# Kernel optimization log

Hardware: AMD Instinct MI355X
Metric: run time of the kernel (lower is better)

## Reference

```python
import jax, jax.numpy as jnp
import numpy as np

N, NFEAT, NHID, NCLASS, NHEADS, E = 4096, 512, 64, 40, 4, 131072
ALPHA = 0.2
NEG = -9e15


def _gat_head(W, b, a, ab, h, adj):
    # Faithful to attention(cat[Wh_i, Wh_j]) but computed without the N*N*2F
    # concat: a . [Wh_i, Wh_j] + ab = (Wh_i . a_src) + (Wh_j . a_dst) + ab
    Wh = h @ W + b                          # [N, F]
    F2 = Wh.shape[1]
    src = Wh @ a[:F2]                       # [N]
    dst = Wh @ a[F2:]                       # [N]
    e = jax.nn.leaky_relu(src[:, None] + dst[None, :] + ab, negative_slope=ALPHA)
    e = jnp.where(adj, e, NEG)              # masked scores [N, N]
    att = jax.nn.softmax(e, axis=1)
    return att @ Wh                         # [N, F]


def setup_inputs() -> dict:
    key = jax.random.key(0)
    ks = jax.random.split(key, 10)
    x = jax.random.normal(ks[0], (N, NFEAT), dtype=jnp.float32)
    edge_index = jax.random.randint(ks[1], (2, E), 0, N, dtype=jnp.int64)
    s = 0.05
    W1 = jax.random.normal(ks[2], (NHEADS, NFEAT, NHID), dtype=jnp.float32) * s
    b1 = jax.random.normal(ks[3], (NHEADS, NHID), dtype=jnp.float32) * s
    a1 = jax.random.normal(ks[4], (NHEADS, 2 * NHID), dtype=jnp.float32) * s
    ab1 = jax.random.normal(ks[5], (NHEADS,), dtype=jnp.float32) * s
    Wo = jax.random.normal(ks[6], (NHEADS * NHID, NCLASS), dtype=jnp.float32) * s
    bo = jax.random.normal(ks[7], (NCLASS,), dtype=jnp.float32) * s
    ao = jax.random.normal(ks[8], (2 * NCLASS,), dtype=jnp.float32) * s
    abo = jax.random.normal(ks[9], (), dtype=jnp.float32) * s
    return {"x": x, "edge_index": edge_index, "W1": W1, "b1": b1, "a1": a1,
            "ab1": ab1, "Wo": Wo, "bo": bo, "ao": ao, "abo": abo}


def reference(x, edge_index, W1, b1, a1, ab1, Wo, bo, ao, abo):
    # dense adjacency from edge list (to_dense_adj equivalent)
    adj = jnp.zeros((N, N), dtype=bool).at[edge_index[0], edge_index[1]].set(True)
    # first multi-head layer (concat=True -> elu per head, then concat)
    hs = jax.vmap(_gat_head, in_axes=(0, 0, 0, 0, None, None))(
        W1, b1, a1, ab1, x, adj)            # [H, N, NHID]
    h = jax.nn.elu(hs)
    h = jnp.transpose(h, (1, 0, 2)).reshape(N, NHEADS * NHID)
    # output head (concat=False), then outer elu + log_softmax
    out = _gat_head(Wo, bo, ao, abo, h, adj)  # [N, NCLASS]
    out = jax.nn.elu(out)
    return jax.nn.log_softmax(out, axis=1)
```

## Files before the change

kernel.cpp:

```cpp
#include <hip/hip_runtime.h>
#include <cstdint>
#include <cstddef>

#define N_NODES 4096
#define NFEAT   512
#define NHID    64
#define NCLASS  40
#define NHEADS  4
#define ALPHA_S 0.2f
#define MAXD    96

typedef __bf16 bf16x8 __attribute__((ext_vector_type(8)));
typedef float  f32x4  __attribute__((ext_vector_type(4)));

__device__ __forceinline__ float lrelu(float x) { return x > 0.f ? x : ALPHA_S * x; }

__device__ __forceinline__ unsigned short f2bf(float f) {
    unsigned u = __float_as_uint(f);
    u += 0x7fffu + ((u >> 16) & 1u);
    return (unsigned short)(u >> 16);
}

__device__ __forceinline__ float wredmax(float m) {
    #pragma unroll
    for (int o = 32; o; o >>= 1) m = fmaxf(m, __shfl_xor(m, o));
    return m;
}
__device__ __forceinline__ float wredsum(float s) {
    #pragma unroll
    for (int o = 32; o; o >>= 1) s += __shfl_xor(s, o);
    return s;
}

__global__ __launch_bounds__(256) void prep(const float* __restrict__ x,
                                            const int* __restrict__ ei, int E,
                                            const float* __restrict__ W1,
                                            const float* __restrict__ Wo,
                                            unsigned short* __restrict__ xb,
                                            unsigned short* __restrict__ Bt,
                                            unsigned short* __restrict__ Wot,
                                            int* __restrict__ cnt,
                                            unsigned short* __restrict__ nbr_raw) {
    const int u = blockIdx.x, tid = threadIdx.x;
    if (u < 1024) {
        size_t idx = (size_t)u * 2048 + tid * 8;
        float4 v0 = *reinterpret_cast<const float4*>(x + idx);
        float4 v1 = *reinterpret_cast<const float4*>(x + idx + 4);
        uint4 o;
        o.x = (unsigned)f2bf(v0.x) | ((unsigned)f2bf(v0.y) << 16);
        o.y = (unsigned)f2bf(v0.z) | ((unsigned)f2bf(v0.w) << 16);
        o.z = (unsigned)f2bf(v1.x) | ((unsigned)f2bf(v1.y) << 16);
        o.w = (unsigned)f2bf(v1.z) | ((unsigned)f2bf(v1.w) << 16);
        *reinterpret_cast<uint4*>(xb + idx) = o;
    } else if (u < 1280) {
        int n = u - 1024;
        int h = n >> 6, c = n & 63;
        for (int k = tid; k < NFEAT; k += 256)
            Bt[(size_t)n * NFEAT + k] = f2bf(W1[(size_t)h * NFEAT * NHID + (size_t)k * NHID + c]);
    } else if (u < 1344) {
        int n = u - 1280;
        unsigned short v = 0;
        if (n < NCLASS) v = f2bf(Wo[(size_t)tid * NCLASS + n]);
        Wot[(size_t)n * 256 + tid] = v;
    } else {
        int t = (u - 1344) * 256 + tid;
        if (t < E) {
            int r = ei[t];
            int c = ei[E + t];
            int slot = atomicAdd(&cnt[r], 1);
            if (slot < MAXD) nbr_raw[(size_t)r * MAXD + slot] = (unsigned short)c;
        }
    }
}

__device__ __forceinline__ void gemm_tile(const unsigned short* __restrict__ Ab,
                                          const unsigned short* __restrict__ Bb,
                                          int K, unsigned short* As, unsigned short* Bs,
                                          f32x4 acc[2][2]) {
    const int tid = threadIdx.x;
    const int l = tid & 63;
    const int wid = tid >> 6;
    const int wr = wid >> 1, wc = wid & 1;
    int aoff[2][2], boff[2][2];
    #pragma unroll
    for (int f = 0; f < 2; ++f) {
        int r = wr * 32 + f * 16 + (l & 15);
        int c = wc * 32 + f * 16 + (l & 15);
        #pragma unroll
        for (int s = 0; s < 2; ++s) {
            int gk = (s << 2) + (l >> 4);
            aoff[f][s] = r * 64 + ((gk ^ (r & 7)) << 3);
            boff[f][s] = c * 64 + ((gk ^ (c & 7)) << 3);
        }
    }
    for (int k0 = 0; k0 < K; k0 += 64) {
        for (int g2 = tid; g2 < 512; g2 += 256) {
            int row = g2 >> 3, gc = g2 & 7;
            uint4 va = *reinterpret_cast<const uint4*>(Ab + (size_t)row * K + k0 + (gc << 3));
            *reinterpret_cast<uint4*>(As + row * 64 + ((gc ^ (row & 7)) << 3)) = va;
            uint4 vb = *reinterpret_cast<const uint4*>(Bb + (size_t)row * K + k0 + (gc << 3));
            *reinterpret_cast<uint4*>(Bs + row * 64 + ((gc ^ (row & 7)) << 3)) = vb;
        }
        __syncthreads();
        #pragma unroll
        for (int s = 0; s < 2; ++s) {
            bf16x8 av[2], bv[2];
            #pragma unroll
            for (int f = 0; f < 2; ++f) {
                av[f] = *reinterpret_cast<const bf16x8*>(As + aoff[f][s]);
                bv[f] = *reinterpret_cast<const bf16x8*>(Bs + boff[f][s]);
            }
            #pragma unroll
            for (int fa = 0; fa < 2; ++fa)
                #pragma unroll
                for (int fb = 0; fb < 2; ++fb)
                    acc[fa][fb] = __builtin_amdgcn_mfma_f32_16x16x32_bf16(
                        av[fa], bv[fb], acc[fa][fb], 0, 0, 0);
        }
        __syncthreads();
    }
}

union MidSMem {
    struct { unsigned short As[4096]; unsigned short Bs[4096]; } g;
    float stage[64][65];
    unsigned int bm[4][128];
};

__global__ __launch_bounds__(256) void mid(const unsigned short* __restrict__ xb,
                                           const unsigned short* __restrict__ Bt,
                                           const float* __restrict__ b1,
                                           const float* __restrict__ a1,
                                           const int* __restrict__ cnt,
                                           const unsigned short* __restrict__ nbr_raw,
                                           float* __restrict__ Wh1,
                                           float* __restrict__ src1,
                                           float* __restrict__ dst1,
                                           int* __restrict__ deg,
                                           unsigned short* __restrict__ nbr) {
    __shared__ MidSMem sm;
    const int tid = threadIdx.x;
    const int l = tid & 63;
    const int wid = tid >> 6;

    if (blockIdx.x < 256) {
        const int u = blockIdx.x;
        const int rt = u & 63, h = u >> 6;
        f32x4 acc[2][2] = {};
        gemm_tile(xb + (size_t)(rt * 64) * NFEAT, Bt + (size_t)(h * 64) * NFEAT,
                  NFEAT, sm.g.As, sm.g.Bs, acc);
        const int wr = wid >> 1, wc = wid & 1;
        #pragma unroll
        for (int fa = 0; fa < 2; ++fa)
            #pragma unroll
            for (int fb = 0; fb < 2; ++fb) {
                int col = wc * 32 + fb * 16 + (l & 15);
                float bias = b1[h * NHID + col];
                #pragma unroll
                for (int j = 0; j < 4; ++j) {
                    int row = wr * 32 + fa * 16 + ((l >> 4) << 2) + j;
                    float v = acc[fa][fb][j] + bias;
                    Wh1[((size_t)h * N_NODES + rt * 64 + row) * NHID + col] = v;
                    sm.stage[row][col] = v;
                }
            }
        __syncthreads();
        for (int rr = 0; rr < 16; ++rr) {
            int row = wid * 16 + rr;
            float v = sm.stage[row][l];
            float s = v * a1[h * 2 * NHID + l];
            float d2 = v * a1[h * 2 * NHID + NHID + l];
            s = wredsum(s); d2 = wredsum(d2);
            if (l == 0) {
                src1[h * N_NODES + rt * 64 + row] = s;
                dst1[h * N_NODES + rt * 64 + row] = d2;
            }
        }
    } else {
        int idx = blockIdx.x - 256;
        for (int u = idx; u < 1024; u += 768) {
            int i = u * 4 + wid;
            sm.bm[wid][2 * l] = 0;
            sm.bm[wid][2 * l + 1] = 0;
            __syncthreads();
            int dr = cnt[i]; if (dr > MAXD) dr = MAXD;
            for (int q = l; q < dr; q += 64) {
                int c = nbr_raw[(size_t)i * MAXD + q];
                atomicOr(&sm.bm[wid][c >> 5], 1u << (c & 31));
            }
            __syncthreads();
            unsigned long long wv = (unsigned long long)sm.bm[wid][2 * l]
                                  | ((unsigned long long)sm.bm[wid][2 * l + 1] << 32);
            int cpc = __popcll(wv);
            int pre = cpc;
            #pragma unroll
            for (int o = 1; o < 64; o <<= 1) {
                int v = __shfl_up(pre, o);
                if (l >= o) pre += v;
            }
            int total = __shfl(pre, 63);
            int basep = pre - cpc;
            if (l == 0) deg[i] = total;
            while (wv) {
                int b = __builtin_ctzll(wv); wv &= wv - 1;
                nbr[(size_t)i * MAXD + basep++] = (unsigned short)(l * 64 + b);
            }
            __syncthreads();
        }
    }
}

__global__ __launch_bounds__(256) void attn1(const float* __restrict__ Wh1,
                                             const float* __restrict__ src1,
                                             const float* __restrict__ dst1,
                                             const float* __restrict__ ab1,
                                             const int* __restrict__ deg,
                                             const unsigned short* __restrict__ nbr,
                                             unsigned short* __restrict__ hb) {
    __shared__ unsigned short nb[MAXD];
    __shared__ float ev[NHEADS][MAXD];
    const int i = blockIdx.x;
    const int tid = threadIdx.x;
    const int l = tid & 63;
    const int h = tid >> 6;
    const int d = deg[i];
    for (int q = tid; q < d; q += 256) nb[q] = nbr[(size_t)i * MAXD + q];
    __syncthreads();
    const float s_i = src1[h * N_NODES + i];
    const float ab = ab1[h];
    const float* __restrict__ dsth = dst1 + h * N_NODES;
    const float* __restrict__ Whh = Wh1 + (size_t)h * N_NODES * NHID;
    int j0 = (l < d) ? nb[l] : -1;
    int j1 = (l + 64 < d) ? nb[l + 64] : -1;
    float s0 = (j0 >= 0) ? lrelu(s_i + dsth[j0] + ab) : -1e30f;
    float s1 = (j1 >= 0) ? lrelu(s_i + dsth[j1] + ab) : -1e30f;
    float m = wredmax(fmaxf(s0, s1));
    float e0 = (j0 >= 0) ? __expf(s0 - m) : 0.f;
    float e1 = (j1 >= 0) ? __expf(s1 - m) : 0.f;
    if (j0 >= 0) ev[h][l] = e0;
    if (j1 >= 0) ev[h][l + 64] = e1;
    float lsum = wredsum(e0 + e1);
    float acc = 0.f;
    if (d == 0) {
        float s = 0.f;
        for (int j = 0; j < N_NODES; ++j) s += Whh[(size_t)j * NHID + l];
        acc = s * (1.f / N_NODES);
    } else {
        #pragma unroll 8
        for (int q = 0; q < d; ++q)
            acc += ev[h][q] * Whh[(size_t)nb[q] * NHID + l];
        acc *= (1.f / lsum);
    }
    float o = acc > 0.f ? acc : __expf(acc) - 1.f;
    hb[(size_t)i * (NHEADS * NHID) + h * NHID + l] = f2bf(o);
}

__global__ __launch_bounds__(256) void gemm2(const unsigned short* __restrict__ hb,
                                             const unsigned short* __restrict__ Wot,
                                             const float* __restrict__ bo,
                                             const float* __restrict__ ao,
                                             float* __restrict__ Who,
                                             float* __restrict__ srco,
                                             float* __restrict__ dsto) {
    __shared__ MidSMem sm;
    const int tid = threadIdx.x;
    const int l = tid & 63;
    const int wid = tid >> 6;
    const int rt = blockIdx.x;
    f32x4 acc[2][2] = {};
    gemm_tile(hb + (size_t)(rt * 64) * (NHEADS * NHID), Wot,
              NHEADS * NHID, sm.g.As, sm.g.Bs, acc);
    const int wr = wid >> 1, wc = wid & 1;
    #pragma unroll
    for (int fa = 0; fa < 2; ++fa)
        #pragma unroll
        for (int fb = 0; fb < 2; ++fb) {
            int col = wc * 32 + fb * 16 + (l & 15);
            if (col < NCLASS) {
                float bias = bo[col];
                #pragma unroll
                for (int j = 0; j < 4; ++j) {
                    int row = wr * 32 + fa * 16 + ((l >> 4) << 2) + j;
                    float v = acc[fa][fb][j] + bias;
                    Who[(size_t)(rt * 64 + row) * NCLASS + col] = v;
                    sm.stage[row][col] = v;
                }
            }
        }
    __syncthreads();
    for (int rr = 0; rr < 16; ++rr) {
        int row = wid * 16 + rr;
        float v = (l < NCLASS) ? sm.stage[row][l] : 0.f;
        float s = (l < NCLASS) ? v * ao[l] : 0.f;
        float d2 = (l < NCLASS) ? v * ao[NCLASS + l] : 0.f;
        s = wredsum(s); d2 = wredsum(d2);
        if (l == 0) {
            srco[rt * 64 + row] = s;
            dsto[rt * 64 + row] = d2;
        }
    }
}

__global__ __launch_bounds__(256) void attn2(const float* __restrict__ Who,
                                             const float* __restrict__ srco,
                                             const float* __restrict__ dsto,
                                             const float* __restrict__ abo_p,
                                             const int* __restrict__ deg,
                                             const unsigned short* __restrict__ nbr,
                                             float* __restrict__ out) {
    __shared__ unsigned short nb[4][MAXD];
    __shared__ float ev[4][MAXD];
    const int tid = threadIdx.x;
    const int wid = tid >> 6;
    const int l = tid & 63;
    const int i = blockIdx.x * 4 + wid;
    const int d = deg[i];
    unsigned short* nbw = nb[wid];
    for (int q = l; q < d; q += 64) nbw[q] = nbr[(size_t)i * MAXD + q];
    const float ab = abo_p[0];
    const float s_i = srco[i];
    int j0 = (l < d) ? nbw[l] : -1;
    int j1 = (l + 64 < d) ? nbw[l + 64] : -1;
    float s0 = (j0 >= 0) ? lrelu(s_i + dsto[j0] + ab) : -1e30f;
    float s1 = (j1 >= 0) ? lrelu(s_i + dsto[j1] + ab) : -1e30f;
    float m = wredmax(fmaxf(s0, s1));
    float e0 = (j0 >= 0) ? __expf(s0 - m) : 0.f;
    float e1 = (j1 >= 0) ? __expf(s1 - m) : 0.f;
    if (j0 >= 0) ev[wid][l] = e0;
    if (j1 >= 0) ev[wid][l + 64] = e1;
    float lsum = wredsum(e0 + e1);
    float acc = 0.f;
    if (d == 0) {
        if (l < NCLASS) {
            float s = 0.f;
            for (int j = 0; j < N_NODES; ++j) s += Who[(size_t)j * NCLASS + l];
            acc = s * (1.f / N_NODES);
        }
    } else if (l < NCLASS) {
        #pragma unroll 8
        for (int q = 0; q < d; ++q)
            acc += ev[wid][q] * Who[(size_t)nbw[q] * NCLASS + l];
        acc *= (1.f / lsum);
    }
    float v = acc > 0.f ? acc : __expf(acc) - 1.f;
    float xv = (l < NCLASS) ? v : -1e30f;
    float mx = wredmax(xv);
    float ex = (l < NCLASS) ? __expf(v - mx) : 0.f;
    ex = wredsum(ex);
    if (l < NCLASS) out[(size_t)i * NCLASS + l] = v - mx - logf(ex);
}

extern "C" void kernel_launch(void* const* d_in, const int* in_sizes, int n_in,
                              void* d_out, int out_size, void* d_ws, size_t ws_size,
                              hipStream_t stream) {
    const float* x   = (const float*)d_in[0];
    const int*   ei  = (const int*)d_in[1];
    const float* W1  = (const float*)d_in[2];
    const float* b1  = (const float*)d_in[3];
    const float* a1  = (const float*)d_in[4];
    const float* ab1 = (const float*)d_in[5];
    const float* Wo  = (const float*)d_in[6];
    const float* bo  = (const float*)d_in[7];
    const float* ao  = (const float*)d_in[8];
    const float* abo = (const float*)d_in[9];
    float* out = (float*)d_out;
    const int E = in_sizes[1] / 2;

    char* base = (char*)d_ws;
    const size_t MB = 1024 * 1024;
    int*            cnt     = (int*)(base);
    int*            deg     = (int*)(base + 16 * 1024);
    unsigned short* nbr_raw = (unsigned short*)(base + 32 * 1024);
    unsigned short* nbr     = (unsigned short*)(base + 32 * 1024 + 786432);
    unsigned short* xb      = (unsigned short*)(base + 2 * MB);
    unsigned short* Bt      = (unsigned short*)(base + 6 * MB);
    unsigned short* Wot     = (unsigned short*)(base + 6 * MB + 262144);
    float*          Wh1     = (float*)(base + 7 * MB);
    float*          src1    = (float*)(base + 11 * MB);
    float*          dst1    = (float*)(base + 11 * MB + 65536);
    unsigned short* hb      = (unsigned short*)(base + 12 * MB);
    float*          Who     = (float*)(base + 14 * MB);
    float*          srco    = (float*)(base + 15 * MB);
    float*          dsto    = (float*)(base + 15 * MB + 16384);

    hipMemsetAsync(cnt, 0, 16 * 1024, stream);
    prep<<<1856, 256, 0, stream>>>(x, ei, E, W1, Wo, xb, Bt, Wot, cnt, nbr_raw);
    mid<<<1024, 256, 0, stream>>>(xb, Bt, b1, a1, cnt, nbr_raw, Wh1, src1, dst1, deg, nbr);
    attn1<<<N_NODES, 256, 0, stream>>>(Wh1, src1, dst1, ab1, deg, nbr, hb);
    gemm2<<<64, 256, 0, stream>>>(hb, Wot, bo, ao, Who, srco, dsto);
    attn2<<<N_NODES / 4, 256, 0, stream>>>(Who, srco, dsto, abo, deg, nbr, out);
}
```

Before: 71.78 us.

## Replace neighbor-list staging with global adjacency bitmask built by atomicOr

Drops the per-row count/raw-neighbor arrays and the separate dedup/compaction pass. A 2 MB dense bitmask is zeroed in prep, and edges are scattered into it with 64-bit atomicOr inside mid, alongside the GEMM blocks. Both attention kernels then rebuild the sorted neighbor list from the bitmask with popcount prefix scans. attn1 also becomes a grid-stride loop over 1024 blocks, and prep handles 16 elements per thread. The cost is zeroing and reading a larger bitmask and repeating the compaction in both attention kernels. MAXD is raised to 128.

```diff
diff --git a/kernel.cpp b/kernel.cpp
--- a/kernel.cpp
+++ b/kernel.cpp
@@ -8,7 +8,7 @@
 #define NCLASS  40
 #define NHEADS  4
 #define ALPHA_S 0.2f
-#define MAXD    96
+#define MAXD    128
 
 typedef __bf16 bf16x8 __attribute__((ext_vector_type(8)));
 typedef float  f32x4  __attribute__((ext_vector_type(4)));
@@ -33,43 +33,40 @@
 }
 
 __global__ __launch_bounds__(256) void prep(const float* __restrict__ x,
-                                            const int* __restrict__ ei, int E,
                                             const float* __restrict__ W1,
                                             const float* __restrict__ Wo,
                                             unsigned short* __restrict__ xb,
                                             unsigned short* __restrict__ Bt,
                                             unsigned short* __restrict__ Wot,
-                                            int* __restrict__ cnt,
-                                            unsigned short* __restrict__ nbr_raw) {
+                                            uint4* __restrict__ adj4) {
     const int u = blockIdx.x, tid = threadIdx.x;
-    if (u < 1024) {
-        size_t idx = (size_t)u * 2048 + tid * 8;
-        float4 v0 = *reinterpret_cast<const float4*>(x + idx);
-        float4 v1 = *reinterpret_cast<const float4*>(x + idx + 4);
-        uint4 o;
-        o.x = (unsigned)f2bf(v0.x) | ((unsigned)f2bf(v0.y) << 16);
-        o.y = (unsigned)f2bf(v0.z) | ((unsigned)f2bf(v0.w) << 16);
-        o.z = (unsigned)f2bf(v1.x) | ((unsigned)f2bf(v1.y) << 16);
-        o.w = (unsigned)f2bf(v1.z) | ((unsigned)f2bf(v1.w) << 16);
-        *reinterpret_cast<uint4*>(xb + idx) = o;
-    } else if (u < 1280) {
-        int n = u - 1024;
+    if (u < 512) {
+        size_t idx = (size_t)u * 4096 + tid * 16;
+        #pragma unroll
+        for (int half = 0; half < 2; ++half) {
+            float4 v0 = *reinterpret_cast<const float4*>(x + idx + half * 8);
+            float4 v1 = *reinterpret_cast<const float4*>(x + idx + half * 8 + 4);
+            uint4 o;
+            o.x = (unsigned)f2bf(v0.x) | ((unsigned)f2bf(v0.y) << 16);
+            o.y = (unsigned)f2bf(v0.z) | ((unsigned)f2bf(v0.w) << 16);
+            o.z = (unsigned)f2bf(v1.x) | ((unsigned)f2bf(v1.y) << 16);
+            o.w = (unsigned)f2bf(v1.z) | ((unsigned)f2bf(v1.w) << 16);
+            *reinterpret_cast<uint4*>(xb + idx + half * 8) = o;
+        }
+    } else if (u < 768) {
+        int n = u - 512;
         int h = n >> 6, c = n & 63;
         for (int k = tid; k < NFEAT; k += 256)
             Bt[(size_t)n * NFEAT + k] = f2bf(W1[(size_t)h * NFEAT * NHID + (size_t)k * NHID + c]);
-    } else if (u < 1344) {
-        int n = u - 1280;
+    } else if (u < 832) {
+        int n = u - 768;
         unsigned short v = 0;
         if (n < NCLASS) v = f2bf(Wo[(size_t)tid * NCLASS + n]);
         Wot[(size_t)n * 256 + tid] = v;
     } else {
-        int t = (u - 1344) * 256 + tid;
-        if (t < E) {
-            int r = ei[t];
-            int c = ei[E + t];
-            int slot = atomicAdd(&cnt[r], 1);
-            if (slot < MAXD) nbr_raw[(size_t)r * MAXD + slot] = (unsigned short)c;
-        }
+        uint4 z = {0, 0, 0, 0};
+        uint4* p = adj4 + (size_t)(u - 832) * 1024 + tid;
+        p[0] = z; p[256] = z; p[512] = z; p[768] = z;
     }
 }
 
@@ -124,20 +121,17 @@
 union MidSMem {
     struct { unsigned short As[4096]; unsigned short Bs[4096]; } g;
     float stage[64][65];
-    unsigned int bm[4][128];
 };
 
 __global__ __launch_bounds__(256) void mid(const unsigned short* __restrict__ xb,
                                            const unsigned short* __restrict__ Bt,
                                            const float* __restrict__ b1,
                                            const float* __restrict__ a1,
-                                           const int* __restrict__ cnt,
-                                           const unsigned short* __restrict__ nbr_raw,
+                                           const int* __restrict__ ei, int E,
+                                           unsigned long long* __restrict__ adj,
                                            float* __restrict__ Wh1,
                                            float* __restrict__ src1,
-                                           float* __restrict__ dst1,
-                                           int* __restrict__ deg,
-                                           unsigned short* __restrict__ nbr) {
+                                           float* __restrict__ dst1) {
     __shared__ MidSMem sm;
     const int tid = threadIdx.x;
     const int l = tid & 63;
@@ -177,82 +171,78 @@
             }
         }
     } else {
-        int idx = blockIdx.x - 256;
-        for (int u = idx; u < 1024; u += 768) {
-            int i = u * 4 + wid;
-            sm.bm[wid][2 * l] = 0;
-            sm.bm[wid][2 * l + 1] = 0;
-            __syncthreads();
-            int dr = cnt[i]; if (dr > MAXD) dr = MAXD;
-            for (int q = l; q < dr; q += 64) {
-                int c = nbr_raw[(size_t)i * MAXD + q];
-                atomicOr(&sm.bm[wid][c >> 5], 1u << (c & 31));
-            }
-            __syncthreads();
-            unsigned long long wv = (unsigned long long)sm.bm[wid][2 * l]
-                                  | ((unsigned long long)sm.bm[wid][2 * l + 1] << 32);
-            int cpc = __popcll(wv);
-            int pre = cpc;
+        int t = (blockIdx.x - 256) * 256 + tid;
+        if (t < E) {
+            int r = ei[t];
+            int c = ei[E + t];
+            atomicOr(&adj[(size_t)r * 64 + (c >> 6)], 1ull << (c & 63));
+        }
+    }
+}
+
+__global__ __launch_bounds__(256) void attn1(const unsigned long long* __restrict__ adj,
+                                             const float* __restrict__ Wh1,
+                                             const float* __restrict__ src1,
+                                             const float* __restrict__ dst1,
+                                             const float* __restrict__ ab1,
+                                             unsigned short* __restrict__ hb) {
+    __shared__ unsigned short nb[MAXD];
+    __shared__ float ev[NHEADS][MAXD];
+    __shared__ int sdeg;
+    const int tid = threadIdx.x;
+    const int l = tid & 63;
+    const int h = tid >> 6;
+
+    for (int i = blockIdx.x; i < N_NODES; i += 1024) {
+        if (h == 0) {
+            unsigned long long w = adj[(size_t)i * 64 + l];
+            int c = __popcll(w);
+            int pre = c;
             #pragma unroll
             for (int o = 1; o < 64; o <<= 1) {
                 int v = __shfl_up(pre, o);
                 if (l >= o) pre += v;
             }
             int total = __shfl(pre, 63);
-            int basep = pre - cpc;
-            if (l == 0) deg[i] = total;
-            while (wv) {
-                int b = __builtin_ctzll(wv); wv &= wv - 1;
-                nbr[(size_t)i * MAXD + basep++] = (unsigned short)(l * 64 + b);
-            }
-            __syncthreads();
-        }
-    }
-}
-
-__global__ __launch_bounds__(256) void attn1(const float* __restrict__ Wh1,
-                                             const float* __restrict__ src1,
-                                             const float* __restrict__ dst1,
-                                             const float* __restrict__ ab1,
-                                             const int* __restrict__ deg,
-                                             const unsigned short* __restrict__ nbr,
-                                             unsigned short* __restrict__ hb) {
-    __shared__ unsigned short nb[MAXD];
-    __shared__ float ev[NHEADS][MAXD];
-    const int i = blockIdx.x;
-    const int tid = threadIdx.x;
-    const int l = tid & 63;
-    const int h = tid >> 6;
-    const int d = deg[i];
-    for (int q = tid; q < d; q += 256) nb[q] = nbr[(size_t)i * MAXD + q];
-    __syncthreads();
-    const float s_i = src1[h * N_NODES + i];
-    const float ab = ab1[h];
-    const float* __restrict__ dsth = dst1 + h * N_NODES;
-    const float* __restrict__ Whh = Wh1 + (size_t)h * N_NODES * NHID;
-    int j0 = (l < d) ? nb[l] : -1;
-    int j1 = (l + 64 < d) ? nb[l + 64] : -1;
-    float s0 = (j0 >= 0) ? lrelu(s_i + dsth[j0] + ab) : -1e30f;
-    float s1 = (j1 >= 0) ? lrelu(s_i + dsth[j1] + ab) : -1e30f;
-    float m = wredmax(fmaxf(s0, s1));
-    float e0 = (j0 >= 0) ? __expf(s0 - m) : 0.f;
-    float e1 = (j1 >= 0) ? __expf(s1 - m) : 0.f;
-    if (j0 >= 0) ev[h][l] = e0;
-    if (j1 >= 0) ev[h][l + 64] = e1;
-    float lsum = wredsum(e0 + e1);
-    float acc = 0.f;
-    if (d == 0) {
-        float s = 0.f;
-        for (int j = 0; j < N_NODES; ++j) s += Whh[(size_t)j * NHID + l];
-        acc = s * (1.f / N_NODES);
-    } else {
-        #pragma unroll 8
-        for (int q = 0; q < d; ++q)
-            acc += ev[h][q] * Whh[(size_t)nb[q] * NHID + l];
-        acc *= (1.f / lsum);
-    }
-    float o = acc > 0.f ? acc : __expf(acc) - 1.f;
-    hb[(size_t)i * (NHEADS * NHID) + h * NHID + l] = f2bf(o);
+            int base = pre - c;
+            if (l == 0) sdeg = total < MAXD ? total : MAXD;
+            while (w) {
+                int b = __builtin_ctzll(w); w &= w - 1;
+                if (base < MAXD) nb[base] = (unsigned short)(l * 64 + b);
+                ++base;
+            }
+        }
+        __syncthreads();
+        const int d = sdeg;
+        const float s_i = src1[h * N_NODES + i];
+        const float ab = ab1[h];
+        const float* __restrict__ dsth = dst1 + h * N_NODES;
+        const float* __restrict__ Whh = Wh1 + (size_t)h * N_NODES * NHID;
+        int j0 = (l < d) ? nb[l] : -1;
+        int j1 = (l + 64 < d) ? nb[l + 64] : -1;
+        float s0 = (j0 >= 0) ? lrelu(s_i + dsth[j0] + ab) : -1e30f;
+        float s1 = (j1 >= 0) ? lrelu(s_i + dsth[j1] + ab) : -1e30f;
+        float m = wredmax(fmaxf(s0, s1));
+        float e0 = (j0 >= 0) ? __expf(s0 - m) : 0.f;
+        float e1 = (j1 >= 0) ? __expf(s1 - m) : 0.f;
+        if (j0 >= 0) ev[h][l] = e0;
+        if (j1 >= 0) ev[h][l + 64] = e1;
+        float lsum = wredsum(e0 + e1);
+        float acc = 0.f;
+        if (d == 0) {
+            float s = 0.f;
+            for (int j = 0; j < N_NODES; ++j) s += Whh[(size_t)j * NHID + l];
+            acc = s * (1.f / N_NODES);
+        } else {
+            #pragma unroll 8
+            for (int q = 0; q < d; ++q)
+                acc += ev[h][q] * Whh[(size_t)nb[q] * NHID + l];
+            acc *= (1.f / lsum);
+        }
+        float o = acc > 0.f ? acc : __expf(acc) - 1.f;
+        hb[(size_t)i * (NHEADS * NHID) + h * NHID + l] = f2bf(o);
+        __syncthreads();
+    }
 }
 
 __global__ __launch_bounds__(256) void gemm2(const unsigned short* __restrict__ hb,
@@ -301,12 +291,11 @@
     }
 }
 
-__global__ __launch_bounds__(256) void attn2(const float* __restrict__ Who,
+__global__ __launch_bounds__(256) void attn2(const unsigned long long* __restrict__ adj,
+                                             const float* __restrict__ Who,
                                              const float* __restrict__ srco,
                                              const float* __restrict__ dsto,
                                              const float* __restrict__ abo_p,
-                                             const int* __restrict__ deg,
-                                             const unsigned short* __restrict__ nbr,
                                              float* __restrict__ out) {
     __shared__ unsigned short nb[4][MAXD];
     __shared__ float ev[4][MAXD];
@@ -314,9 +303,25 @@
     const int wid = tid >> 6;
     const int l = tid & 63;
     const int i = blockIdx.x * 4 + wid;
-    const int d = deg[i];
     unsigned short* nbw = nb[wid];
-    for (int q = l; q < d; q += 64) nbw[q] = nbr[(size_t)i * MAXD + q];
+
+    unsigned long long w = adj[(size_t)i * 64 + l];
+    int c = __popcll(w);
+    int pre = c;
+    #pragma unroll
+    for (int o = 1; o < 64; o <<= 1) {
+        int v = __shfl_up(pre, o);
+        if (l >= o) pre += v;
+    }
+    int total = __shfl(pre, 63);
+    int base = pre - c;
+    const int d = total < MAXD ? total : MAXD;
+    while (w) {
+        int b = __builtin_ctzll(w); w &= w - 1;
+        if (base < MAXD) nbw[base] = (unsigned short)(l * 64 + b);
+        ++base;
+    }
+
     const float ab = abo_p[0];
     const float s_i = srco[i];
     int j0 = (l < d) ? nbw[l] : -1;
@@ -368,10 +373,7 @@
 
     char* base = (char*)d_ws;
     const size_t MB = 1024 * 1024;
-    int*            cnt     = (int*)(base);
-    int*            deg     = (int*)(base + 16 * 1024);
-    unsigned short* nbr_raw = (unsigned short*)(base + 32 * 1024);
-    unsigned short* nbr     = (unsigned short*)(base + 32 * 1024 + 786432);
+    unsigned long long* adj = (unsigned long long*)(base);
     unsigned short* xb      = (unsigned short*)(base + 2 * MB);
     unsigned short* Bt      = (unsigned short*)(base + 6 * MB);
     unsigned short* Wot     = (unsigned short*)(base + 6 * MB + 262144);
@@ -383,10 +385,10 @@
     float*          srco    = (float*)(base + 15 * MB);
     float*          dsto    = (float*)(base + 15 * MB + 16384);
 
-    hipMemsetAsync(cnt, 0, 16 * 1024, stream);
-    prep<<<1856, 256, 0, stream>>>(x, ei, E, W1, Wo, xb, Bt, Wot, cnt, nbr_raw);
-    mid<<<1024, 256, 0, stream>>>(xb, Bt, b1, a1, cnt, nbr_raw, Wh1, src1, dst1, deg, nbr);
-    attn1<<<N_NODES, 256, 0, stream>>>(Wh1, src1, dst1, ab1, deg, nbr, hb);
+    prep<<<960, 256, 0, stream>>>(x, W1, Wo, xb, Bt, Wot, (uint4*)adj);
+    mid<<<256 + (E + 255) / 256, 256, 0, stream>>>(xb, Bt, b1, a1, ei, E, adj,
+                                                   Wh1, src1, dst1);
+    attn1<<<1024, 256, 0, stream>>>(adj, Wh1, src1, dst1, ab1, hb);
     gemm2<<<64, 256, 0, stream>>>(hb, Wot, bo, ao, Who, srco, dsto);
-    attn2<<<N_NODES / 4, 256, 0, stream>>>(Who, srco, dsto, abo, deg, nbr, out);
-}
+    attn2<<<N_NODES / 4, 256, 0, stream>>>(adj, Who, srco, dsto, abo, out);
+}
```

New measurement: 69.37 us. 1.03x faster.
